# Performance work log

Hardware: AMD Instinct MI355X
Metric: run time of the kernel (lower is better)

## Reference

```python
import math
import jax, jax.numpy as jnp
import numpy as np

D_MODEL = 1024
NUM_SCALES = 4
STATE_SIZE = 16
EXPAND = 2
D_INNER = D_MODEL * EXPAND
D_PER_SCALE = D_INNER // NUM_SCALES
BATCH, SEQ = 4, 4096


def _make_A_log():
    base = np.arange(1, STATE_SIZE + 1, dtype=np.float32)  # (N,)
    parts = [np.broadcast_to(base * (2.0 ** i), (D_PER_SCALE, STATE_SIZE)) for i in range(NUM_SCALES)]
    A = np.concatenate(parts, axis=0)  # (d_inner, N)
    return jnp.asarray(np.log(A))


def setup_inputs() -> dict:
    key = jax.random.key(0)
    ks = jax.random.split(key, 8)
    scale = 0.02
    x = jax.random.normal(ks[0], (BATCH, SEQ, D_MODEL), dtype=jnp.float32)
    W_in = jax.random.normal(ks[1], (2 * D_INNER, D_MODEL), dtype=jnp.float32) * scale
    W_B = jax.random.normal(ks[2], (STATE_SIZE, D_INNER), dtype=jnp.float32) * scale
    W_C = jax.random.normal(ks[3], (STATE_SIZE, D_INNER), dtype=jnp.float32) * scale
    W_dt = jax.random.normal(ks[4], (D_INNER, D_INNER), dtype=jnp.float32) * scale
    # dt bias: log of dt_init ~ Uniform in log-space between 1e-3 and 1e-1
    u = jax.random.uniform(ks[5], (D_INNER,), dtype=jnp.float32)
    b_dt = u * (math.log(0.1) - math.log(0.001)) + math.log(0.001)
    W_out = jax.random.normal(ks[6], (D_MODEL, D_INNER), dtype=jnp.float32) * scale
    A_log = _make_A_log()
    D = jnp.ones((D_INNER,), dtype=jnp.float32)
    output_gate = jnp.zeros((1,), dtype=jnp.float32)
    return {"x": x, "W_in": W_in, "A_log": A_log, "W_B": W_B, "W_C": W_C,
            "W_dt": W_dt, "b_dt": b_dt, "D": D, "output_gate": output_gate, "W_out": W_out}


def _selective_scan(x_ssm, A, B_mat, C_mat, dt):
    # x_ssm: (B,L,d), A: (d,N), B_mat/C_mat: (B,L,N), dt: (B,L,d)
    b, L, d = x_ssm.shape
    N = A.shape[1]
    h0 = jnp.zeros((b, d, N), dtype=jnp.float32)

    def step(h, inp):
        dt_t, B_t, C_t, x_t = inp  # (B,d),(B,N),(B,N),(B,d)
        A_bar = jnp.exp(jnp.minimum(dt_t[..., None] * A, 20.0))       # (B,d,N)
        B_bar = dt_t[..., None] * B_t[:, None, :]                      # (B,d,N)
        h = A_bar * h + B_bar * x_t[..., None]
        y_t = jnp.einsum('bdn,bn->bd', h, C_t)
        return h, y_t

    xs = (jnp.swapaxes(dt, 0, 1), jnp.swapaxes(B_mat, 0, 1),
          jnp.swapaxes(C_mat, 0, 1), jnp.swapaxes(x_ssm, 0, 1))
    _, ys = jax.lax.scan(step, h0, xs)   # ys: (L,B,d)
    return jnp.swapaxes(ys, 0, 1)


def reference(x, W_in, A_log, W_B, W_C, W_dt, b_dt, D, output_gate, W_out):
    xz = jnp.einsum('bld,ed->ble', x, W_in)          # (B,L,2*d_inner)
    x_ssm, z = jnp.split(xz, 2, axis=-1)
    A = -jnp.exp(A_log.astype(jnp.float32))           # (d_inner,N)
    B_mat = jnp.einsum('bld,nd->bln', x_ssm, W_B)
    C_mat = jnp.einsum('bld,nd->bln', x_ssm, W_C)
    dt = jax.nn.softplus(jnp.einsum('bld,ed->ble', x_ssm, W_dt) + b_dt)
    y = _selective_scan(x_ssm.astype(jnp.float32), A,
                        B_mat.astype(jnp.float32), C_mat.astype(jnp.float32),
                        dt.astype(jnp.float32))
    y = y + x_ssm * D[None, None, :]
    y = y * jax.nn.silu(z)
    out = jnp.einsum('ble,de->bld', y, W_out) * jax.nn.sigmoid(output_gate)
    return out
```

## Files before the change

### kernel.cpp

```cpp
#include <hip/hip_runtime.h>
#include <hip/hip_bf16.h>
#include <math.h>

#define D_MODEL 1024
#define D_INNER 2048
#define NSTATE  16
#define BATCH   4
#define SEQ     4096
#define MTOT    (BATCH*SEQ)
#define SDT     2176
#define NCAT    2176
#define NCHUNK  16
#define CLEN    (SEQ/NCHUNK)
#define N1      (2*D_INNER)

typedef __attribute__((ext_vector_type(8))) __bf16 bf16x8;
typedef __attribute__((ext_vector_type(4))) float f32x4;

__device__ __forceinline__ float b2f(unsigned short u){
  return __uint_as_float(((unsigned int)u) << 16);
}
__device__ __forceinline__ unsigned short f2b(float f){
  unsigned int u = __float_as_uint(f);
  u = (u + 0x7FFFu + ((u >> 16) & 1u)) >> 16;
  return (unsigned short)u;
}
__device__ __forceinline__ float softplus_f(float x){
  float r = log1pf(__expf(-fabsf(x)));
  return x > 0.f ? x + r : r;
}

__global__ void cvt_f2b_kernel(const float* __restrict__ src,
                               unsigned short* __restrict__ dst){
  int i = (blockIdx.x * 256 + threadIdx.x) * 4;
  float4 v = *(const float4*)(src + i);
  ushort2 lo = {f2b(v.x), f2b(v.y)};
  ushort2 hi = {f2b(v.z), f2b(v.w)};
  *(ushort2*)(dst + i)     = lo;
  *(ushort2*)(dst + i + 2) = hi;
}

__global__ void concat_w_kernel(const float* __restrict__ Wdt,
                                const float* __restrict__ WB,
                                const float* __restrict__ WC,
                                unsigned short* __restrict__ Wcat){
  int idx = blockIdx.x * 256 + threadIdx.x;
  int row = idx >> 9;
  int q   = idx & 511;
  float4 v;
  if      (row < 2048) v = *(const float4*)(Wdt + ((size_t)row * 2048 + q * 4));
  else if (row < 2064) v = *(const float4*)(WB  + ((size_t)(row - 2048) * 2048 + q * 4));
  else if (row < 2080) v = *(const float4*)(WC  + ((size_t)(row - 2064) * 2048 + q * 4));
  else                 v = make_float4(0.f, 0.f, 0.f, 0.f);
  unsigned short* p = Wcat + (size_t)idx * 4;
  *(ushort2*)(p)     = (ushort2){f2b(v.x), f2b(v.y)};
  *(ushort2*)(p + 2) = (ushort2){f2b(v.z), f2b(v.w)};
}

template<int MODE, int AF32>
__global__ __launch_bounds__(256) void gemm_bt(
    const void* __restrict__ Av,
    const unsigned short* __restrict__ W,
    unsigned short* __restrict__ o0,
    unsigned short* __restrict__ o1,
    float* __restrict__ of,
    const float* __restrict__ bias,
    int K)
{
  const int bm = blockIdx.y, bn = blockIdx.x;
  const int tid = threadIdx.x;
  const int lane = tid & 63;
  const int wid = tid >> 6;
  const int wr = wid >> 1, wc = wid & 1;

  __shared__ unsigned short sA[128 * 72];
  __shared__ unsigned short sB[128 * 72];

  f32x4 acc[4][4];
  #pragma unroll
  for (int i = 0; i < 4; i++)
    #pragma unroll
    for (int j = 0; j < 4; j++) acc[i][j] = (f32x4){0.f, 0.f, 0.f, 0.f};

  const int lrow = tid >> 3;
  const int lch  = tid & 7;
  const unsigned short* Ab = (const unsigned short*)Av + (size_t)(bm * 128 + lrow) * K + lch * 8;
  const float*          Af = (const float*)Av          + (size_t)(bm * 128 + lrow) * K + lch * 8;
  const unsigned short* Wp = W + (size_t)(bn * 128 + lrow) * K + lch * 8;

  for (int k0 = 0; k0 < K; k0 += 64) {
    #pragma unroll
    for (int i = 0; i < 4; i++) {
      uint4 va;
      if (AF32) {
        float4 f0 = *(const float4*)(Af + (size_t)(i * 32) * K + k0);
        float4 f1 = *(const float4*)(Af + (size_t)(i * 32) * K + k0 + 4);
        va.x = (unsigned int)f2b(f0.x) | ((unsigned int)f2b(f0.y) << 16);
        va.y = (unsigned int)f2b(f0.z) | ((unsigned int)f2b(f0.w) << 16);
        va.z = (unsigned int)f2b(f1.x) | ((unsigned int)f2b(f1.y) << 16);
        va.w = (unsigned int)f2b(f1.z) | ((unsigned int)f2b(f1.w) << 16);
      } else {
        va = *(const uint4*)(Ab + (size_t)(i * 32) * K + k0);
      }
      uint4 vb = *(const uint4*)(Wp + (size_t)(i * 32) * K + k0);
      *(uint4*)&sA[(lrow + i * 32) * 72 + lch * 8] = va;
      *(uint4*)&sB[(lrow + i * 32) * 72 + lch * 8] = vb;
    }
    __syncthreads();
    #pragma unroll
    for (int kk = 0; kk < 2; kk++) {
      const int kb = kk * 32 + (lane >> 4) * 8;
      bf16x8 af[4], bfr[4];
      #pragma unroll
      for (int mt = 0; mt < 4; mt++)
        af[mt] = *(const bf16x8*)&sA[(wr * 64 + mt * 16 + (lane & 15)) * 72 + kb];
      #pragma unroll
      for (int nt = 0; nt < 4; nt++)
        bfr[nt] = *(const bf16x8*)&sB[(wc * 64 + nt * 16 + (lane & 15)) * 72 + kb];
      #pragma unroll
      for (int mt = 0; mt < 4; mt++)
        #pragma unroll
        for (int nt = 0; nt < 4; nt++)
          acc[mt][nt] = __builtin_amdgcn_mfma_f32_16x16x32_bf16(
              af[mt], bfr[nt], acc[mt][nt], 0, 0, 0);
    }
    __syncthreads();
  }

  float gscale = 1.f;
  if (MODE == 2) {
    gscale = 1.f / (1.f + __expf(-bias[0]));
  }

  const int r0 = bm * 128 + wr * 64 + ((lane >> 4) << 2);
  const int c0 = bn * 128 + wc * 64 + (lane & 15);
  #pragma unroll
  for (int mt = 0; mt < 4; mt++) {
    #pragma unroll
    for (int nt = 0; nt < 4; nt++) {
      const int col = c0 + nt * 16;
      #pragma unroll
      for (int i = 0; i < 4; i++) {
        const int row = r0 + mt * 16 + i;
        float v = acc[mt][nt][i];
        if (MODE == 0) {
          if (col < D_INNER) o0[(size_t)row * D_INNER + col] = f2b(v);
          else               o1[(size_t)row * D_INNER + (col - D_INNER)] = f2b(v);
        } else if (MODE == 1) {
          if (col < D_INNER) v = softplus_f(v + bias[col]);
          o0[(size_t)row * SDT + col] = f2b(v);
        } else {
          of[(size_t)row * D_MODEL + col] = v * gscale;
        }
      }
    }
  }
}

__global__ __launch_bounds__(256) void scan_passA(
    const unsigned short* __restrict__ dtBC,
    const unsigned short* __restrict__ xs,
    const float* __restrict__ Alog,
    float* __restrict__ Pb, float* __restrict__ Sb)
{
  const int d = blockIdx.x * 256 + threadIdx.x;
  const int b = blockIdx.y;
  const int c = blockIdx.z;

  float a[NSTATE];
  #pragma unroll
  for (int n = 0; n < NSTATE; n++) a[n] = -__expf(Alog[d * NSTATE + n]);

  float P[NSTATE], S[NSTATE];
  #pragma unroll
  for (int n = 0; n < NSTATE; n++) { P[n] = 1.f; S[n] = 0.f; }

  __shared__ float sB[16][16];
  const size_t bL = (size_t)b * SEQ;
  const int t0c = c * CLEN;
  const int lt = threadIdx.x >> 4, ln = threadIdx.x & 15;

  for (int t0 = t0c; t0 < t0c + CLEN; t0 += 16) {
    __syncthreads();
    sB[lt][ln] = b2f(dtBC[(bL + t0 + lt) * SDT + 2048 + ln]);
    __syncthreads();
    for (int tt = 0; tt < 16; tt++) {
      const size_t rw = bL + t0 + tt;
      const float dt = b2f(dtBC[rw * SDT + d]);
      const float x  = b2f(xs[rw * D_INNER + d]);
      const float dtx = dt * x;
      #pragma unroll
      for (int n = 0; n < NSTATE; n++) {
        const float ab = __expf(dt * a[n]);
        P[n] *= ab;
        S[n] = ab * S[n] + dtx * sB[tt][n];
      }
    }
  }
  const size_t base = (((size_t)c * BATCH + b) * D_INNER + d) * NSTATE;
  #pragma unroll
  for (int n = 0; n < NSTATE; n += 4) {
    *(f32x4*)&Pb[base + n] = (f32x4){P[n], P[n+1], P[n+2], P[n+3]};
    *(f32x4*)&Sb[base + n] = (f32x4){S[n], S[n+1], S[n+2], S[n+3]};
  }
}

__global__ __launch_bounds__(256) void scan_passB(float* __restrict__ Pb,
                                                  const float* __restrict__ Sb)
{
  const size_t j = (size_t)blockIdx.x * 256 + threadIdx.x;
  const size_t stride = (size_t)BATCH * D_INNER * NSTATE;
  float h = 0.f;
  for (int c = 0; c < NCHUNK; c++) {
    const size_t idx = (size_t)c * stride + j;
    const float p = Pb[idx];
    const float s = Sb[idx];
    Pb[idx] = h;
    h = p * h + s;
  }
}

__global__ __launch_bounds__(256) void scan_passC(
    const unsigned short* __restrict__ dtBC,
    const unsigned short* __restrict__ xs,
    const unsigned short* __restrict__ zb,
    const float* __restrict__ Alog,
    const float* __restrict__ Dv,
    const float* __restrict__ Hb,
    unsigned short* __restrict__ yb)
{
  const int d = blockIdx.x * 256 + threadIdx.x;
  const int b = blockIdx.y;
  const int c = blockIdx.z;

  float a[NSTATE];
  #pragma unroll
  for (int n = 0; n < NSTATE; n++) a[n] = -__expf(Alog[d * NSTATE + n]);

  float h[NSTATE];
  const size_t base = (((size_t)c * BATCH + b) * D_INNER + d) * NSTATE;
  #pragma unroll
  for (int n = 0; n < NSTATE; n += 4) {
    f32x4 v = *(const f32x4*)&Hb[base + n];
    h[n] = v.x; h[n+1] = v.y; h[n+2] = v.z; h[n+3] = v.w;
  }
  const float Dd = Dv[d];

  __shared__ float sB[16][16];
  __shared__ float sC[16][16];
  const size_t bL = (size_t)b * SEQ;
  const int t0c = c * CLEN;
  const int lt = threadIdx.x >> 4, ln = threadIdx.x & 15;

  for (int t0 = t0c; t0 < t0c + CLEN; t0 += 16) {
    __syncthreads();
    {
      const size_t rwb = (bL + t0 + lt) * SDT + 2048;
      sB[lt][ln] = b2f(dtBC[rwb + ln]);
      sC[lt][ln] = b2f(dtBC[rwb + 16 + ln]);
    }
    __syncthreads();
    for (int tt = 0; tt < 16; tt++) {
      const size_t rw = bL + t0 + tt;
      const float dt = b2f(dtBC[rw * SDT + d]);
      const float x  = b2f(xs[rw * D_INNER + d]);
      const float z  = b2f(zb[rw * D_INNER + d]);
      const float dtx = dt * x;
      float y = 0.f;
      #pragma unroll
      for (int n = 0; n < NSTATE; n++) {
        const float ab = __expf(dt * a[n]);
        h[n] = ab * h[n] + dtx * sB[tt][n];
        y += h[n] * sC[tt][n];
      }
      y = (y + x * Dd) * (z / (1.f + __expf(-z)));
      yb[rw * D_INNER + d] = f2b(y);
    }
  }
}

extern "C" void kernel_launch(void* const* d_in, const int* in_sizes, int n_in,
                              void* d_out, int out_size, void* d_ws, size_t ws_size,
                              hipStream_t stream)
{
  const float* x    = (const float*)d_in[0];
  const float* Win  = (const float*)d_in[1];
  const float* Alog = (const float*)d_in[2];
  const float* WB   = (const float*)d_in[3];
  const float* WC   = (const float*)d_in[4];
  const float* Wdt  = (const float*)d_in[5];
  const float* bdt  = (const float*)d_in[6];
  const float* Dv   = (const float*)d_in[7];
  const float* gate = (const float*)d_in[8];
  const float* Wout = (const float*)d_in[9];
  float* outp = (float*)d_out;

  char* ws = (char*)d_ws;
  unsigned short* xs    = (unsigned short*)(ws + 0);
  unsigned short* zy    = (unsigned short*)(ws + 67108864);
  unsigned short* dtBC  = (unsigned short*)(ws + 134217728);
  unsigned short* Woutb = (unsigned short*)(ws + 205520896);

  char* ob = (char*)d_out;
  float* Pb = (float*)(ob + 0);
  float* Sb = (float*)(ob + 8388608);
  unsigned short* Winb  = (unsigned short*)(ob + 16777216);
  unsigned short* Wcatb = (unsigned short*)(ob + 25165824);

  cvt_f2b_kernel<<<4096, 256, 0, stream>>>(Win, Winb);
  cvt_f2b_kernel<<<2048, 256, 0, stream>>>(Wout, Woutb);
  concat_w_kernel<<<4352, 256, 0, stream>>>(Wdt, WB, WC, Wcatb);

  gemm_bt<0, 1><<<dim3(N1 / 128, MTOT / 128), 256, 0, stream>>>(
      (const void*)x, Winb, xs, zy, nullptr, nullptr, D_MODEL);
  gemm_bt<1, 0><<<dim3(NCAT / 128, MTOT / 128), 256, 0, stream>>>(
      (const void*)xs, Wcatb, dtBC, nullptr, nullptr, bdt, D_INNER);
  scan_passA<<<dim3(D_INNER / 256, BATCH, NCHUNK), 256, 0, stream>>>(
      dtBC, xs, Alog, Pb, Sb);
  scan_passB<<<(BATCH * D_INNER * NSTATE) / 256, 256, 0, stream>>>(Pb, Sb);
  scan_passC<<<dim3(D_INNER / 256, BATCH, NCHUNK), 256, 0, stream>>>(
      dtBC, xs, zy, Alog, Dv, Pb, zy);
  gemm_bt<2, 0><<<dim3(D_MODEL / 128, MTOT / 128), 256, 0, stream>>>(
      (const void*)zy, Woutb, nullptr, nullptr, outp, gate, D_INNER);
}
```

Measured before the change: 1.262 ms.

## Use direct global-to-LDS async loads with XOR swizzle in bf16 GEMMs

The GEMM tiles now load straight from global memory into LDS with global_load_lds instead of staging through registers. The padded LDS layout is replaced by an XOR-swizzled 64-wide layout so the MFMA fragment reads avoid bank conflicts. Because the direct path cannot convert types, x is converted to bf16 in a separate pre-pass and Winb moves into the workspace. This trades an extra x conversion kernel and more scratch buffers for cheaper tile loads in all three GEMMs.

Result: faster. 1.148 ms (-9.0%).

```diff
diff --git a/kernel.cpp b/kernel.cpp
--- a/kernel.cpp
+++ b/kernel.cpp
@@ -30,14 +30,18 @@
   return x > 0.f ? x + r : r;
 }
 
+__device__ __forceinline__ void async16(unsigned short* lds, const unsigned short* g){
+  __builtin_amdgcn_global_load_lds(
+      (const __attribute__((address_space(1))) unsigned int*)g,
+      (__attribute__((address_space(3))) unsigned int*)lds, 16, 0, 0);
+}
+
 __global__ void cvt_f2b_kernel(const float* __restrict__ src,
                                unsigned short* __restrict__ dst){
   int i = (blockIdx.x * 256 + threadIdx.x) * 4;
   float4 v = *(const float4*)(src + i);
-  ushort2 lo = {f2b(v.x), f2b(v.y)};
-  ushort2 hi = {f2b(v.z), f2b(v.w)};
-  *(ushort2*)(dst + i)     = lo;
-  *(ushort2*)(dst + i + 2) = hi;
+  *(ushort2*)(dst + i)     = (ushort2){f2b(v.x), f2b(v.y)};
+  *(ushort2*)(dst + i + 2) = (ushort2){f2b(v.z), f2b(v.w)};
 }
 
 __global__ void concat_w_kernel(const float* __restrict__ Wdt,
@@ -57,9 +61,9 @@
   *(ushort2*)(p + 2) = (ushort2){f2b(v.z), f2b(v.w)};
 }
 
-template<int MODE, int AF32>
+template<int MODE>
 __global__ __launch_bounds__(256) void gemm_bt(
-    const void* __restrict__ Av,
+    const unsigned short* __restrict__ A,
     const unsigned short* __restrict__ W,
     unsigned short* __restrict__ o0,
     unsigned short* __restrict__ o1,
@@ -70,11 +74,11 @@
   const int bm = blockIdx.y, bn = blockIdx.x;
   const int tid = threadIdx.x;
   const int lane = tid & 63;
-  const int wid = tid >> 6;
-  const int wr = wid >> 1, wc = wid & 1;
-
-  __shared__ unsigned short sA[128 * 72];
-  __shared__ unsigned short sB[128 * 72];
+  const int w = tid >> 6;
+  const int wr = w >> 1, wc = w & 1;
+
+  __shared__ unsigned short sA[128 * 64];
+  __shared__ unsigned short sB[128 * 64];
 
   f32x4 acc[4][4];
   #pragma unroll
@@ -82,41 +86,36 @@
     #pragma unroll
     for (int j = 0; j < 4; j++) acc[i][j] = (f32x4){0.f, 0.f, 0.f, 0.f};
 
-  const int lrow = tid >> 3;
-  const int lch  = tid & 7;
-  const unsigned short* Ab = (const unsigned short*)Av + (size_t)(bm * 128 + lrow) * K + lch * 8;
-  const float*          Af = (const float*)Av          + (size_t)(bm * 128 + lrow) * K + lch * 8;
-  const unsigned short* Wp = W + (size_t)(bn * 128 + lrow) * K + lch * 8;
+  const int rw8 = lane >> 3;
+  const int ch  = (lane & 7) ^ rw8;
+  const unsigned short* Ag = A + (size_t)(bm * 128 + w * 32 + rw8) * K + ch * 8;
+  const unsigned short* Wg = W + (size_t)(bn * 128 + w * 32 + rw8) * K + ch * 8;
+  unsigned short* sAw = &sA[(w * 32) * 64];
+  unsigned short* sBw = &sB[(w * 32) * 64];
+
+  const int m16 = lane & 15, q = lane >> 4;
 
   for (int k0 = 0; k0 < K; k0 += 64) {
     #pragma unroll
-    for (int i = 0; i < 4; i++) {
-      uint4 va;
-      if (AF32) {
-        float4 f0 = *(const float4*)(Af + (size_t)(i * 32) * K + k0);
-        float4 f1 = *(const float4*)(Af + (size_t)(i * 32) * K + k0 + 4);
-        va.x = (unsigned int)f2b(f0.x) | ((unsigned int)f2b(f0.y) << 16);
-        va.y = (unsigned int)f2b(f0.z) | ((unsigned int)f2b(f0.w) << 16);
-        va.z = (unsigned int)f2b(f1.x) | ((unsigned int)f2b(f1.y) << 16);
-        va.w = (unsigned int)f2b(f1.z) | ((unsigned int)f2b(f1.w) << 16);
-      } else {
-        va = *(const uint4*)(Ab + (size_t)(i * 32) * K + k0);
-      }
-      uint4 vb = *(const uint4*)(Wp + (size_t)(i * 32) * K + k0);
-      *(uint4*)&sA[(lrow + i * 32) * 72 + lch * 8] = va;
-      *(uint4*)&sB[(lrow + i * 32) * 72 + lch * 8] = vb;
-    }
+    for (int it = 0; it < 4; it++)
+      async16(sAw + it * 8 * 64, Ag + (size_t)(it * 8) * K + k0);
+    #pragma unroll
+    for (int it = 0; it < 4; it++)
+      async16(sBw + it * 8 * 64, Wg + (size_t)(it * 8) * K + k0);
     __syncthreads();
     #pragma unroll
     for (int kk = 0; kk < 2; kk++) {
-      const int kb = kk * 32 + (lane >> 4) * 8;
       bf16x8 af[4], bfr[4];
       #pragma unroll
-      for (int mt = 0; mt < 4; mt++)
-        af[mt] = *(const bf16x8*)&sA[(wr * 64 + mt * 16 + (lane & 15)) * 72 + kb];
-      #pragma unroll
-      for (int nt = 0; nt < 4; nt++)
-        bfr[nt] = *(const bf16x8*)&sB[(wc * 64 + nt * 16 + (lane & 15)) * 72 + kb];
+      for (int mt = 0; mt < 4; mt++) {
+        const int row = wr * 64 + mt * 16 + m16;
+        af[mt] = *(const bf16x8*)&sA[row * 64 + (((kk * 4 + q) ^ (m16 & 7)) << 3)];
+      }
+      #pragma unroll
+      for (int nt = 0; nt < 4; nt++) {
+        const int row = wc * 64 + nt * 16 + m16;
+        bfr[nt] = *(const bf16x8*)&sB[row * 64 + (((kk * 4 + q) ^ (m16 & 7)) << 3)];
+      }
       #pragma unroll
       for (int mt = 0; mt < 4; mt++)
         #pragma unroll
@@ -128,12 +127,10 @@
   }
 
   float gscale = 1.f;
-  if (MODE == 2) {
-    gscale = 1.f / (1.f + __expf(-bias[0]));
-  }
-
-  const int r0 = bm * 128 + wr * 64 + ((lane >> 4) << 2);
-  const int c0 = bn * 128 + wc * 64 + (lane & 15);
+  if (MODE == 2) gscale = 1.f / (1.f + __expf(-bias[0]));
+
+  const int r0 = bm * 128 + wr * 64 + (q << 2);
+  const int c0 = bn * 128 + wc * 64 + m16;
   #pragma unroll
   for (int mt = 0; mt < 4; mt++) {
     #pragma unroll
@@ -299,27 +296,29 @@
   unsigned short* xs    = (unsigned short*)(ws + 0);
   unsigned short* zy    = (unsigned short*)(ws + 67108864);
   unsigned short* dtBC  = (unsigned short*)(ws + 134217728);
-  unsigned short* Woutb = (unsigned short*)(ws + 205520896);
+  unsigned short* Winb  = (unsigned short*)(ws + 205520896);
+  unsigned short* Woutb = (unsigned short*)(ws + 213909504);
 
   char* ob = (char*)d_out;
   float* Pb = (float*)(ob + 0);
   float* Sb = (float*)(ob + 8388608);
-  unsigned short* Winb  = (unsigned short*)(ob + 16777216);
-  unsigned short* Wcatb = (unsigned short*)(ob + 25165824);
-
+  unsigned short* Wcatb = (unsigned short*)(ob + 16777216);
+  unsigned short* xb    = (unsigned short*)(ob + 33554432);
+
+  cvt_f2b_kernel<<<16384, 256, 0, stream>>>(x, xb);
   cvt_f2b_kernel<<<4096, 256, 0, stream>>>(Win, Winb);
   cvt_f2b_kernel<<<2048, 256, 0, stream>>>(Wout, Woutb);
   concat_w_kernel<<<4352, 256, 0, stream>>>(Wdt, WB, WC, Wcatb);
 
-  gemm_bt<0, 1><<<dim3(N1 / 128, MTOT / 128), 256, 0, stream>>>(
-      (const void*)x, Winb, xs, zy, nullptr, nullptr, D_MODEL);
-  gemm_bt<1, 0><<<dim3(NCAT / 128, MTOT / 128), 256, 0, stream>>>(
-      (const void*)xs, Wcatb, dtBC, nullptr, nullptr, bdt, D_INNER);
+  gemm_bt<0><<<dim3(N1 / 128, MTOT / 128), 256, 0, stream>>>(
+      xb, Winb, xs, zy, nullptr, nullptr, D_MODEL);
+  gemm_bt<1><<<dim3(NCAT / 128, MTOT / 128), 256, 0, stream>>>(
+      xs, Wcatb, dtBC, nullptr, nullptr, bdt, D_INNER);
   scan_passA<<<dim3(D_INNER / 256, BATCH, NCHUNK), 256, 0, stream>>>(
       dtBC, xs, Alog, Pb, Sb);
   scan_passB<<<(BATCH * D_INNER * NSTATE) / 256, 256, 0, stream>>>(Pb, Sb);
   scan_passC<<<dim3(D_INNER / 256, BATCH, NCHUNK), 256, 0, stream>>>(
       dtBC, xs, zy, Alog, Dv, Pb, zy);
-  gemm_bt<2, 0><<<dim3(D_MODEL / 128, MTOT / 128), 256, 0, stream>>>(
-      (const void*)zy, Woutb, nullptr, nullptr, outp, gate, D_INNER);
-}
+  gemm_bt<2><<<dim3(D_MODEL / 128, MTOT / 128), 256, 0, stream>>>(
+      zy, Woutb, nullptr, nullptr, outp, gate, D_INNER);
+}
```
